# Performance work log

Measured on AMD Instinct MI355X. Metric: run time of the kernel, lower is better.

## Reference

```python
import jax, jax.numpy as jnp
import numpy as np

NUM_FEATURES = 128   # conv spatial length
WINDOW = 128         # conv channels / lstm seq len
KC = 16              # kernels per group
KS = 3               # conv kernel size
FC1 = 32             # number of independent LSTMs
H = 32               # lstm hidden size
NL = 2               # lstm layers
PAD = 1
POOL_LEN = (NUM_FEATURES + 2 * PAD) // 2  # maxpool(k=2,s=2,p=1) output length
B = 128


def setup_inputs():
    key = jax.random.key(0)
    ks = jax.random.split(key, 13)
    x = jax.random.normal(ks[0], (B, WINDOW, NUM_FEATURES), jnp.float32)
    conv_w = jax.random.normal(ks[1], (WINDOW * KC, 1, KS), jnp.float32) * 0.3
    conv_b = jax.random.normal(ks[2], (WINDOW * KC,), jnp.float32) * 0.1
    fc1_in = KC * POOL_LEN
    fc1_w = jax.random.normal(ks[3], (FC1, fc1_in), jnp.float32) * 0.02
    fc1_b = jax.random.normal(ks[4], (FC1,), jnp.float32) * 0.02
    w_ih0 = jax.random.normal(ks[5], (FC1, 4 * H), jnp.float32) * 0.1          # layer0, input size 1
    w_ih1 = jax.random.normal(ks[6], (NL - 1, FC1, 4 * H, H), jnp.float32) * 0.1
    w_hh = jax.random.normal(ks[7], (NL, FC1, 4 * H, H), jnp.float32) * 0.1
    b_lstm = jax.random.normal(ks[8], (NL, FC1, 4 * H), jnp.float32) * 0.1     # bias_ih + bias_hh combined
    mu_w = jax.random.normal(ks[9], (1, FC1 * H), jnp.float32) * 0.05
    mu_b = jax.random.normal(ks[10], (1,), jnp.float32) * 0.05
    lv_w = jax.random.normal(ks[11], (1, FC1 * H), jnp.float32) * 0.05
    lv_b = jax.random.normal(ks[12], (1,), jnp.float32) * 0.05
    return {"x": x, "conv_w": conv_w, "conv_b": conv_b, "fc1_w": fc1_w, "fc1_b": fc1_b,
            "w_ih0": w_ih0, "w_ih1": w_ih1, "w_hh": w_hh, "b_lstm": b_lstm,
            "mu_w": mu_w, "mu_b": mu_b, "lv_w": lv_w, "lv_b": lv_b}


def _lstm_cell(gates, c_prev):
    # torch gate order: i, f, g, o
    i, f, g, o = jnp.split(gates, 4, axis=-1)
    c_new = jax.nn.sigmoid(f) * c_prev + jax.nn.sigmoid(i) * jnp.tanh(g)
    h_new = jax.nn.sigmoid(o) * jnp.tanh(c_new)
    return h_new, c_new


def reference(x, conv_w, conv_b, fc1_w, fc1_b, w_ih0, w_ih1, w_hh, b_lstm, mu_w, mu_b, lv_w, lv_b):
    bsz = x.shape[0]
    # grouped conv1d: groups = WINDOW, each group maps 1 -> KC channels
    y = jax.lax.conv_general_dilated(x, conv_w, window_strides=(1,), padding=[(PAD, PAD)],
                                     feature_group_count=WINDOW,
                                     dimension_numbers=('NCH', 'OIH', 'NCH'))
    y = jax.nn.relu(y + conv_b[None, :, None])
    neg = jnp.finfo(y.dtype).min
    y = jnp.pad(y, ((0, 0), (0, 0), (PAD, PAD)), constant_values=neg)
    y = y.reshape(bsz, WINDOW * KC, POOL_LEN, 2).max(axis=-1)
    # regroup to [B, WINDOW, KC*POOL_LEN] (channel layout = group-major, matches torch view)
    y = y.reshape(bsz, WINDOW, KC * POOL_LEN)
    z = jnp.einsum('bwi,oi->bwo', y, fc1_w) + fc1_b   # [B, WINDOW, FC1]

    # FC1 independent NL-layer LSTMs batched over the feature axis; time axis = WINDOW
    h0 = jnp.zeros((NL, bsz, FC1, H), z.dtype)
    c0 = jnp.zeros_like(h0)

    def step(carry, x_t):  # x_t: [B, FC1]
        h, c = carry
        hs, cs = [], []
        gates = jnp.einsum('bf,fg->bfg', x_t, w_ih0) + jnp.einsum('bfh,fgh->bfg', h[0], w_hh[0]) + b_lstm[0]
        h_l, c_l = _lstm_cell(gates, c[0])
        hs.append(h_l); cs.append(c_l)
        for l in range(1, NL):
            gates = (jnp.einsum('bfh,fgh->bfg', h_l, w_ih1[l - 1])
                     + jnp.einsum('bfh,fgh->bfg', h[l], w_hh[l]) + b_lstm[l])
            h_l, c_l = _lstm_cell(gates, c[l])
            hs.append(h_l); cs.append(c_l)
        return (jnp.stack(hs), jnp.stack(cs)), None

    (h_fin, _), _ = jax.lax.scan(step, (h0, c0), jnp.transpose(z, (1, 0, 2)))
    combined = h_fin[-1].reshape(bsz, FC1 * H)  # top layer, last step; feature-major like torch.cat
    mu = combined @ mu_w.T + mu_b
    log_var = combined @ lv_w.T + lv_b
    sigma = jnp.exp(0.5 * log_var)
    return (mu - 1.96 * sigma, mu, mu + 1.96 * sigma, log_var)
```

## Files before the change

### kernel.cpp

```cpp
#include <hip/hip_runtime.h>
#include <hip/hip_bf16.h>
#include <math.h>

#define BATCH 128
#define WIN   128
#define NF    128
#define KC    16
#define POOL  65
#define NFC1  32
#define HS    32
#define LW    40
#define KP    1056
#define PSTR  1064

typedef float f32x4 __attribute__((ext_vector_type(4)));
typedef short bf16x8 __attribute__((ext_vector_type(8)));

#define LOG2E   1.442695041f
#define LOG2E2  2.885390082f

__device__ __forceinline__ float cellf(float& c, float gi, float gf, float gg, float go) {
    float ei = __builtin_amdgcn_exp2f(gi);
    float ef = __builtin_amdgcn_exp2f(gf);
    float eg = __builtin_amdgcn_exp2f(gg);
    float eo = __builtin_amdgcn_exp2f(go);
    float sf = __builtin_amdgcn_rcpf(1.f + ef);
    c = fmaf(sf, c, (eg - 1.f) * __builtin_amdgcn_rcpf((1.f + ei) * (eg + 1.f)));
    float ec = __builtin_amdgcn_exp2f(__builtin_amdgcn_fmed3f(c, -30.f, 30.f) * LOG2E2);
    return (ec - 1.f) * __builtin_amdgcn_rcpf((1.f + eo) * (ec + 1.f));
}
__device__ __forceinline__ unsigned short f2bf(float x) {
    __hip_bfloat16 h = __float2bfloat16(x);
    unsigned short u; __builtin_memcpy(&u, &h, 2); return u;
}
__device__ __forceinline__ float bf2f(unsigned short u) {
    unsigned int v = ((unsigned int)u) << 16;
    float f; __builtin_memcpy(&f, &v, 4); return f;
}
__device__ __forceinline__ bf16x8 load_row8_scaled(const float* row, float sc) {
    float4 lo = ((const float4*)row)[0];
    float4 hi = ((const float4*)row)[1];
    union { bf16x8 v; unsigned short u[8]; } t;
    t.u[0] = f2bf(lo.x * sc); t.u[1] = f2bf(lo.y * sc); t.u[2] = f2bf(lo.z * sc); t.u[3] = f2bf(lo.w * sc);
    t.u[4] = f2bf(hi.x * sc); t.u[5] = f2bf(hi.y * sc); t.u[6] = f2bf(hi.z * sc); t.u[7] = f2bf(hi.w * sc);
    return t.v;
}

__global__ __launch_bounds__(256) void k0_wconv(
    const float* __restrict__ fc1_w, unsigned short* __restrict__ w_bf)
{
    const int o = blockIdx.x;
    for (int i = threadIdx.x; i < KP; i += 256) {
        float v = (i < KC * POOL) ? fc1_w[(size_t)o * (KC * POOL) + i] : 0.f;
        w_bf[(size_t)o * KP + i] = f2bf(v);
    }
}

__global__ __launch_bounds__(256, 4) void k1_conv_fc1(
    const float* __restrict__ x, const float* __restrict__ conv_w, const float* __restrict__ conv_b,
    const unsigned short* __restrict__ w_bf, const float* __restrict__ fc1_b, float* __restrict__ z)
{
    __shared__ __align__(16) unsigned short xp[16][132];
    __shared__ __align__(16) unsigned short poolb[16 * PSTR];
    __shared__ float cw[KC][3];
    __shared__ float cb[KC];
    __shared__ float fb[NFC1];

    const int w = blockIdx.x >> 3;
    const int bbase = (blockIdx.x & 7) * 16;
    const int tid = threadIdx.x;

    if (tid < KC * 3) cw[tid / 3][tid % 3] = conv_w[(w * KC + tid / 3) * 3 + tid % 3];
    if (tid >= 64 && tid < 64 + KC) cb[tid - 64] = conv_b[w * KC + (tid - 64)];
    if (tid >= 96 && tid < 96 + NFC1) fb[tid - 96] = fc1_b[tid - 96];

    for (int i = tid; i < 16 * 32; i += 256) {
        int b = i >> 5, q = i & 31;
        float4 v = ((const float4*)(x + (size_t)(bbase + b) * (WIN * NF) + (size_t)w * NF))[q];
        unsigned short* dst = &xp[b][1 + q * 4];
        dst[0] = f2bf(v.x); dst[1] = f2bf(v.y); dst[2] = f2bf(v.z); dst[3] = f2bf(v.w);
    }
    if (tid < 16) { xp[tid][0] = 0; xp[tid][129] = 0; xp[tid][130] = 0; xp[tid][131] = 0; }
    __syncthreads();

    {
        const int b = tid >> 4;
        const int k = tid & 15;
        const float w0 = cw[k][0], w1 = cw[k][1], w2 = cw[k][2], bb = cb[k];
        float v1 = 0.f;
        float v2 = bf2f(xp[b][0]);
        float v3 = bf2f(xp[b][1]);
        unsigned short* prow = &poolb[b * PSTR + k * POOL];
        #pragma unroll 5
        for (int j = 0; j < POOL; ++j) {
            float v0 = v1; v1 = v2; v2 = v3;
            v3 = bf2f(xp[b][2 * j + 2]);
            float oa = bb + w0 * v0 + w1 * v1 + w2 * v2;
            float ob = bb + w0 * v1 + w1 * v2 + w2 * v3;
            float m = 0.f;
            if (j > 0)        m = fmaxf(m, oa);
            if (j < POOL - 1) m = fmaxf(m, ob);
            prow[j] = f2bf(m);
        }
    }
    for (int i = tid; i < 16 * (KP - KC * POOL); i += 256) {
        int b = i >> 4, c = i & 15;
        poolb[b * PSTR + KC * POOL + c] = 0;
    }
    __syncthreads();

    const int lane = tid & 63;
    const int wid = tid >> 6;
    if (wid < 2) {
        const int col = lane & 15;
        const int kg = lane >> 4;
        const int g = wid * 16 + col;
        f32x4 acc;
        {
            float bias = fb[g];
            acc[0] = bias; acc[1] = bias; acc[2] = bias; acc[3] = bias;
        }
        const unsigned short* wrow = w_bf + (size_t)g * KP;
        #pragma unroll 4
        for (int ks = 0; ks < KP / 32; ++ks) {
            bf16x8 aP = *(const bf16x8*)&poolb[col * PSTR + ks * 32 + kg * 8];
            bf16x8 bW = *(const bf16x8*)&wrow[ks * 32 + kg * 8];
            acc = __builtin_amdgcn_mfma_f32_16x16x32_bf16(aP, bW, acc, 0, 0, 0);
        }
        float4 st; st.x = acc[0]; st.y = acc[1]; st.z = acc[2]; st.w = acc[3];
        *(float4*)&z[(size_t)w * (NFC1 * BATCH) + (size_t)g * BATCH + bbase + kg * 4] = st;
    }
}

__global__ __launch_bounds__(256, 1) void k2_lstm_mfma(
    const float* __restrict__ w_ih0, const float* __restrict__ w_ih1,
    const float* __restrict__ w_hh, const float* __restrict__ b_lstm,
    const float* __restrict__ mu_w, const float* __restrict__ lv_w,
    const float* __restrict__ z, float* __restrict__ pm, float* __restrict__ pl)
{
    __shared__ float zs[WIN][16];
    __shared__ __align__(16) unsigned short h0b0[16 * LW];
    __shared__ __align__(16) unsigned short h0b1[16 * LW];
    __shared__ __align__(16) unsigned short h1b0[16 * LW];
    __shared__ __align__(16) unsigned short h1b1[16 * LW];

    const int f = blockIdx.x >> 3;
    const int bbase = (blockIdx.x & 7) * 16;
    const int tid = threadIdx.x;
    const int wid = tid >> 6, lane = tid & 63;
    const bool isL0 = (wid < 2);
    const int s = wid & 1;
    const int col = lane & 15;
    const int kg = lane >> 4;

    for (int i = tid; i < WIN * 4; i += 256) {
        int t = i >> 2, q = i & 3;
        ((float4*)&zs[t][0])[q] = ((const float4*)&z[(size_t)t * (NFC1 * BATCH) + f * BATCH + bbase])[q];
    }
    for (int i = tid; i < 16 * LW; i += 256) {
        h0b0[i] = 0; h0b1[i] = 0; h1b0[i] = 0; h1b1[i] = 0;
    }

    const float gsc[4] = { -LOG2E, -LOG2E, LOG2E2, -LOG2E };

    const float* WA = isL0 ? (w_hh + (size_t)f * 4096)
                           : (w_ih1 + (size_t)f * 4096);
    const float* WV = w_hh + (size_t)(NFC1 + f) * 4096;
    bf16x8 fA[4], fB[4];
    float bias[4], wi0[4];
    float mw = 0.f, lw = 0.f;
    const int loff = isL0 ? 0 : (NFC1 * 128);
    #pragma unroll
    for (int gi = 0; gi < 4; ++gi) {
        int nt = gi * 2 + s;
        int g = nt * 16 + col;
        fA[gi] = load_row8_scaled(WA + g * 32 + kg * 8, gsc[gi]);
        if (!isL0) fB[gi] = load_row8_scaled(WV + g * 32 + kg * 8, gsc[gi]);
        bias[gi] = b_lstm[loff + f * 128 + g] * gsc[gi];
        wi0[gi] = w_ih0[f * 128 + g] * gsc[gi];
    }
    if (!isL0) {
        mw = mu_w[f * HS + 16 * s + col];
        lw = lv_w[f * HS + 16 * s + col];
    }
    __syncthreads();

    const int hread = col * LW + kg * 8;
    const int hw0 = (kg * 4 + 0) * LW + 16 * s + col;
    float cst[4] = {0.f, 0.f, 0.f, 0.f};
    f32x4 zv = *(const f32x4*)&zs[0][kg * 4];

    auto body = [&](int it, const unsigned short* h0r, unsigned short* h0w,
                            const unsigned short* h1r, unsigned short* h1w) {
        if (isL0) {
            if (it < WIN) {
                bf16x8 hA = *(const bf16x8*)&h0r[hread];
                f32x4 aI, aF, aG, aO;
                #pragma unroll
                for (int j = 0; j < 4; ++j) {
                    aI[j] = fmaf(zv[j], wi0[0], bias[0]);
                    aF[j] = fmaf(zv[j], wi0[1], bias[1]);
                    aG[j] = fmaf(zv[j], wi0[2], bias[2]);
                    aO[j] = fmaf(zv[j], wi0[3], bias[3]);
                }
                aI = __builtin_amdgcn_mfma_f32_16x16x32_bf16(hA, fA[0], aI, 0, 0, 0);
                aF = __builtin_amdgcn_mfma_f32_16x16x32_bf16(hA, fA[1], aF, 0, 0, 0);
                aG = __builtin_amdgcn_mfma_f32_16x16x32_bf16(hA, fA[2], aG, 0, 0, 0);
                aO = __builtin_amdgcn_mfma_f32_16x16x32_bf16(hA, fA[3], aO, 0, 0, 0);
                if (it + 1 < WIN) zv = *(const f32x4*)&zs[it + 1][kg * 4];
                #pragma unroll
                for (int j = 0; j < 4; ++j) {
                    float h = cellf(cst[j], aI[j], aF[j], aG[j], aO[j]);
                    h0w[hw0 + j * LW] = f2bf(h);
                }
            }
        } else {
            if (it >= 1) {
                bf16x8 hA = *(const bf16x8*)&h0r[hread];
                bf16x8 hB = *(const bf16x8*)&h1r[hread];
                f32x4 aI, aF, aG, aO;
                #pragma unroll
                for (int j = 0; j < 4; ++j) { aI[j] = bias[0]; aF[j] = bias[1]; aG[j] = bias[2]; aO[j] = bias[3]; }
                aI = __builtin_amdgcn_mfma_f32_16x16x32_bf16(hA, fA[0], aI, 0, 0, 0);
                aI = __builtin_amdgcn_mfma_f32_16x16x32_bf16(hB, fB[0], aI, 0, 0, 0);
                aF = __builtin_amdgcn_mfma_f32_16x16x32_bf16(hA, fA[1], aF, 0, 0, 0);
                aF = __builtin_amdgcn_mfma_f32_16x16x32_bf16(hB, fB[1], aF, 0, 0, 0);
                aG = __builtin_amdgcn_mfma_f32_16x16x32_bf16(hA, fA[2], aG, 0, 0, 0);
                aG = __builtin_amdgcn_mfma_f32_16x16x32_bf16(hB, fB[2], aG, 0, 0, 0);
                aO = __builtin_amdgcn_mfma_f32_16x16x32_bf16(hA, fA[3], aO, 0, 0, 0);
                aO = __builtin_amdgcn_mfma_f32_16x16x32_bf16(hB, fB[3], aO, 0, 0, 0);
                if (it < WIN) {
                    #pragma unroll
                    for (int j = 0; j < 4; ++j) {
                        float h = cellf(cst[j], aI[j], aF[j], aG[j], aO[j]);
                        h1w[hw0 + j * LW] = f2bf(h);
                    }
                } else {
                    f32x4 pmv, plv;
                    #pragma unroll
                    for (int j = 0; j < 4; ++j) {
                        float h = cellf(cst[j], aI[j], aF[j], aG[j], aO[j]);
                        pmv[j] = h * mw;
                        plv[j] = h * lw;
                    }
                    #pragma unroll
                    for (int m = 1; m < 16; m <<= 1) {
                        #pragma unroll
                        for (int j = 0; j < 4; ++j) {
                            pmv[j] += __shfl_xor(pmv[j], m, 64);
                            plv[j] += __shfl_xor(plv[j], m, 64);
                        }
                    }
                    if (col == 0) {
                        #pragma unroll
                        for (int j = 0; j < 4; ++j) {
                            pm[(size_t)(f * 2 + s) * BATCH + bbase + kg * 4 + j] = pmv[j];
                            pl[(size_t)(f * 2 + s) * BATCH + bbase + kg * 4 + j] = plv[j];
                        }
                    }
                }
            }
        }
    };

    body(0, h0b0, h0b1, h1b0, h1b1);
    __syncthreads();
    #pragma unroll 1
    for (int it = 1; it <= WIN; it += 2) {
        body(it,     h0b1, h0b0, h1b1, h1b0);
        __syncthreads();
        body(it + 1, h0b0, h0b1, h1b0, h1b1);
        __syncthreads();
    }
}

__global__ __launch_bounds__(128) void k3_head(
    const float* __restrict__ pm, const float* __restrict__ pl,
    const float* __restrict__ mu_b, const float* __restrict__ lv_b, float* __restrict__ out)
{
    const int b = threadIdx.x;
    float am = mu_b[0], al = lv_b[0];
    #pragma unroll 8
    for (int i = 0; i < 2 * NFC1; ++i) {
        am += pm[i * BATCH + b];
        al += pl[i * BATCH + b];
    }
    float sg = __expf(0.5f * al);
    out[b]           = am - 1.96f * sg;
    out[128 + b]     = am;
    out[256 + b]     = am + 1.96f * sg;
    out[384 + b]     = al;
}

extern "C" void kernel_launch(void* const* d_in, const int* in_sizes, int n_in,
                              void* d_out, int out_size, void* d_ws, size_t ws_size,
                              hipStream_t stream)
{
    const float* x      = (const float*)d_in[0];
    const float* conv_w = (const float*)d_in[1];
    const float* conv_b = (const float*)d_in[2];
    const float* fc1_w  = (const float*)d_in[3];
    const float* fc1_b  = (const float*)d_in[4];
    const float* w_ih0  = (const float*)d_in[5];
    const float* w_ih1  = (const float*)d_in[6];
    const float* w_hh   = (const float*)d_in[7];
    const float* b_lstm = (const float*)d_in[8];
    const float* mu_w   = (const float*)d_in[9];
    const float* mu_b   = (const float*)d_in[10];
    const float* lv_w   = (const float*)d_in[11];
    const float* lv_b   = (const float*)d_in[12];
    float* out = (float*)d_out;

    float* z  = (float*)d_ws;
    float* pm = z + (size_t)WIN * NFC1 * BATCH;
    float* pl = pm + (size_t)2 * NFC1 * BATCH;
    unsigned short* w_bf = (unsigned short*)(z + 524288 + 131072);

    k0_wconv<<<dim3(NFC1), dim3(256), 0, stream>>>(fc1_w, w_bf);
    k1_conv_fc1<<<dim3(WIN * 8), dim3(256), 0, stream>>>(x, conv_w, conv_b, w_bf, fc1_b, z);
    k2_lstm_mfma<<<dim3(NFC1 * 8), dim3(256), 0, stream>>>(w_ih0, w_ih1, w_hh, b_lstm,
                                                           mu_w, lv_w, z, pm, pl);
    k3_head<<<dim3(1), dim3(128), 0, stream>>>(pm, pl, mu_b, lv_b, out);
}
```

Before: 83.26 us.

## Fold fc1 weight bf16 conversion into conv kernel and double block threads

Removes the separate k0 kernel that converted fc1_w to padded bf16. The conv/fc1 kernel now reads fp32 weights directly and converts them inline, zero-filling the padded tail. The block grows to 512 threads, and each thread handles half of the pooled outputs for one (batch, kernel) pair. This saves a kernel launch and a global round trip, but every block now redoes the weight conversion, and the larger block may lower occupancy.

```diff
diff --git a/kernel.cpp b/kernel.cpp
--- a/kernel.cpp
+++ b/kernel.cpp
@@ -37,6 +37,14 @@
     unsigned int v = ((unsigned int)u) << 16;
     float f; __builtin_memcpy(&f, &v, 4); return f;
 }
+__device__ __forceinline__ bf16x8 load_row8(const float* row) {
+    float4 lo = ((const float4*)row)[0];
+    float4 hi = ((const float4*)row)[1];
+    union { bf16x8 v; unsigned short u[8]; } t;
+    t.u[0] = f2bf(lo.x); t.u[1] = f2bf(lo.y); t.u[2] = f2bf(lo.z); t.u[3] = f2bf(lo.w);
+    t.u[4] = f2bf(hi.x); t.u[5] = f2bf(hi.y); t.u[6] = f2bf(hi.z); t.u[7] = f2bf(hi.w);
+    return t.v;
+}
 __device__ __forceinline__ bf16x8 load_row8_scaled(const float* row, float sc) {
     float4 lo = ((const float4*)row)[0];
     float4 hi = ((const float4*)row)[1];
@@ -46,19 +54,9 @@
     return t.v;
 }
 
-__global__ __launch_bounds__(256) void k0_wconv(
-    const float* __restrict__ fc1_w, unsigned short* __restrict__ w_bf)
-{
-    const int o = blockIdx.x;
-    for (int i = threadIdx.x; i < KP; i += 256) {
-        float v = (i < KC * POOL) ? fc1_w[(size_t)o * (KC * POOL) + i] : 0.f;
-        w_bf[(size_t)o * KP + i] = f2bf(v);
-    }
-}
-
-__global__ __launch_bounds__(256, 4) void k1_conv_fc1(
+__global__ __launch_bounds__(512, 4) void k1_conv_fc1(
     const float* __restrict__ x, const float* __restrict__ conv_w, const float* __restrict__ conv_b,
-    const unsigned short* __restrict__ w_bf, const float* __restrict__ fc1_b, float* __restrict__ z)
+    const float* __restrict__ fc1_w, const float* __restrict__ fc1_b, float* __restrict__ z)
 {
     __shared__ __align__(16) unsigned short xp[16][132];
     __shared__ __align__(16) unsigned short poolb[16 * PSTR];
@@ -74,8 +72,8 @@
     if (tid >= 64 && tid < 64 + KC) cb[tid - 64] = conv_b[w * KC + (tid - 64)];
     if (tid >= 96 && tid < 96 + NFC1) fb[tid - 96] = fc1_b[tid - 96];
 
-    for (int i = tid; i < 16 * 32; i += 256) {
-        int b = i >> 5, q = i & 31;
+    {
+        int b = tid >> 5, q = tid & 31;
         float4 v = ((const float4*)(x + (size_t)(bbase + b) * (WIN * NF) + (size_t)w * NF))[q];
         unsigned short* dst = &xp[b][1 + q * 4];
         dst[0] = f2bf(v.x); dst[1] = f2bf(v.y); dst[2] = f2bf(v.z); dst[3] = f2bf(v.w);
@@ -84,15 +82,18 @@
     __syncthreads();
 
     {
-        const int b = tid >> 4;
-        const int k = tid & 15;
+        const int b = tid >> 5;
+        const int k = (tid >> 1) & 15;
+        const int jh = tid & 1;
+        const int j0 = jh * 33;
+        const int jend = jh ? POOL : 33;
         const float w0 = cw[k][0], w1 = cw[k][1], w2 = cw[k][2], bb = cb[k];
-        float v1 = 0.f;
-        float v2 = bf2f(xp[b][0]);
-        float v3 = bf2f(xp[b][1]);
+        float v1 = jh ? bf2f(xp[b][2 * j0 - 1]) : 0.f;
+        float v2 = bf2f(xp[b][2 * j0]);
+        float v3 = bf2f(xp[b][2 * j0 + 1]);
         unsigned short* prow = &poolb[b * PSTR + k * POOL];
         #pragma unroll 5
-        for (int j = 0; j < POOL; ++j) {
+        for (int j = j0; j < jend; ++j) {
             float v0 = v1; v1 = v2; v2 = v3;
             v3 = bf2f(xp[b][2 * j + 2]);
             float oa = bb + w0 * v0 + w1 * v1 + w2 * v2;
@@ -103,7 +104,7 @@
             prow[j] = f2bf(m);
         }
     }
-    for (int i = tid; i < 16 * (KP - KC * POOL); i += 256) {
+    for (int i = tid; i < 16 * (KP - KC * POOL); i += 512) {
         int b = i >> 4, c = i & 15;
         poolb[b * PSTR + KC * POOL + c] = 0;
     }
@@ -120,11 +121,14 @@
             float bias = fb[g];
             acc[0] = bias; acc[1] = bias; acc[2] = bias; acc[3] = bias;
         }
-        const unsigned short* wrow = w_bf + (size_t)g * KP;
+        const float* wrow = fc1_w + (size_t)g * (KC * POOL);
         #pragma unroll 4
         for (int ks = 0; ks < KP / 32; ++ks) {
-            bf16x8 aP = *(const bf16x8*)&poolb[col * PSTR + ks * 32 + kg * 8];
-            bf16x8 bW = *(const bf16x8*)&wrow[ks * 32 + kg * 8];
+            const int koff = ks * 32 + kg * 8;
+            bf16x8 aP = *(const bf16x8*)&poolb[col * PSTR + koff];
+            bf16x8 bW;
+            if (koff < KC * POOL) bW = load_row8(wrow + koff);
+            else                  bW = (bf16x8){0, 0, 0, 0, 0, 0, 0, 0};
             acc = __builtin_amdgcn_mfma_f32_16x16x32_bf16(aP, bW, acc, 0, 0, 0);
         }
         float4 st; st.x = acc[0]; st.y = acc[1]; st.z = acc[2]; st.w = acc[3];
@@ -314,10 +318,8 @@
     float* z  = (float*)d_ws;
     float* pm = z + (size_t)WIN * NFC1 * BATCH;
     float* pl = pm + (size_t)2 * NFC1 * BATCH;
-    unsigned short* w_bf = (unsigned short*)(z + 524288 + 131072);
-
-    k0_wconv<<<dim3(NFC1), dim3(256), 0, stream>>>(fc1_w, w_bf);
-    k1_conv_fc1<<<dim3(WIN * 8), dim3(256), 0, stream>>>(x, conv_w, conv_b, w_bf, fc1_b, z);
+
+    k1_conv_fc1<<<dim3(WIN * 8), dim3(512), 0, stream>>>(x, conv_w, conv_b, fc1_w, fc1_b, z);
     k2_lstm_mfma<<<dim3(NFC1 * 8), dim3(256), 0, stream>>>(w_ih0, w_ih1, w_hh, b_lstm,
                                                            mu_w, lv_w, z, pm, pl);
     k3_head<<<dim3(1), dim3(128), 0, stream>>>(pm, pl, mu_b, lv_b, out);
```

Result: slower. 85.97 us (+3.3%).
